# Kernel tuning notes

Hardware: AMD Instinct MI355X
Metric: run time of the kernel (lower is better)

Reference implementation:

```python
import jax, jax.numpy as jnp
import numpy as np

B, S, H = 64, 2048, 768
LAM = 0.0  # sparsegen-lin lambda (lam=0 -> sparsemax)
NEG = -1e30


def setup_inputs() -> dict:
    key = jax.random.key(0)
    k1, k2, k3, k4, k5 = jax.random.split(key, 5)
    hidden = jax.random.normal(k1, (B, S, H), jnp.float32)
    # contiguous entity spans of random length (>=16 valid tokens per example)
    lengths = jax.random.randint(k2, (B,), 16, S)
    mask1d = (jnp.arange(S)[None, :] < lengths[:, None]).astype(jnp.float32)
    token_mask = jnp.broadcast_to(mask1d[:, :, None], (B, S, H))
    pooled_tokens = jax.random.normal(k3, (B, H), jnp.float32)
    w_align = jax.random.normal(k4, (2 * H,), jnp.float32) * 0.02
    b_align = jax.random.normal(k5, (1,), jnp.float32) * 0.02
    return {"hidden": hidden, "token_mask": token_mask,
            "pooled_tokens": pooled_tokens, "w_align": w_align, "b_align": b_align}


def sparsegen_masked(scores, valid, lam):
    """Batched sparsegen-lin over valid positions only.
    scores: [B, S] float, valid: [B, S] bool. Returns probs [B, S] (0 at invalid).
    Matches per-example torch SparsegenLin applied to masked_select'd scores.
    """
    n = scores.shape[-1]
    zmax = jnp.max(jnp.where(valid, scores, -jnp.inf), axis=-1, keepdims=True)
    z = scores - zmax                                # subtract max over valid
    z_sortable = jnp.where(valid, z, NEG)
    zs = -jnp.sort(-z_sortable, axis=-1)             # descending; valid first
    n_valid = jnp.sum(valid, axis=-1, keepdims=True)
    ks = jnp.arange(1, n + 1, dtype=scores.dtype)[None, :]
    sorted_valid = ks <= n_valid.astype(scores.dtype)
    zs_m = jnp.where(sorted_valid, zs, 0.0)
    csum = jnp.cumsum(zs_m, axis=-1)
    bound = 1.0 - lam + ks * zs_m
    is_gt = (bound > csum) & sorted_valid
    k = jnp.maximum(jnp.max(jnp.where(is_gt, ks, 0.0), axis=-1, keepdims=True), 1.0)
    tau = (jnp.sum(jnp.where(is_gt, zs_m, 0.0), axis=-1, keepdims=True) - 1.0 + lam) / k
    ps = jnp.maximum((z - tau) / (1.0 - lam), 0.0)
    return jnp.where(valid, ps, 0.0)


def reference(hidden, token_mask, pooled_tokens, w_align, b_align):
    masked_hidden = hidden * token_mask                       # [B,S,H]
    tokens_rep_masked = pooled_tokens[:, None, :] * token_mask  # [B,S,H]
    # alignment_model(cat(tokens_rep_masked, masked_hidden)) -> [B,S]
    scores = (jnp.einsum('bsh,h->bs', tokens_rep_masked, w_align[:H])
              + jnp.einsum('bsh,h->bs', masked_hidden, w_align[H:])
              + b_align[0])
    attn_mask = token_mask[:, :, 0] > 0                       # [B,S] bool
    attention_probs = sparsegen_masked(scores, attn_mask, LAM)[:, :, None]  # [B,S,1]
    pooled = jnp.sum(masked_hidden * attention_probs, axis=1)  # [B,H]
    # insize == outsize -> output_layer is skipped (projected = pooled)
    return pooled, attention_probs
```

## Files before the change

### kernel.cpp

```cpp
#include <hip/hip_runtime.h>
#include <hip/hip_bf16.h>
#include <cstdint>
#include <cstddef>

#define BB 64
#define SS 2048
#define HH 768
#define LAM 0.0f
#define NEGV -1e30f

__global__ void lengths_kernel(const float* __restrict__ token_mask,
                               int* __restrict__ lens) {
    int wv = threadIdx.x >> 6;
    int b = blockIdx.x * 16 + wv;
    int lane = threadIdx.x & 63;

    int s1 = lane * 32;
    bool m1 = token_mask[((size_t)b * SS + s1) * HH] > 0.f;
    unsigned long long bal1 = __ballot(m1);
    int cnt1 = (int)__popcll(bal1);
    int base = (cnt1 - 1) * 32;

    int s2 = base + 1 + (lane & 31);
    if (s2 > SS - 1) s2 = SS - 1;
    bool m2 = token_mask[((size_t)b * SS + s2) * HH] > 0.f;
    unsigned long long bal2 = __ballot(m2) & 0xFFFFFFFFull;
    int cnt2 = (int)__popcll(bal2);
    if (lane == 0) lens[b] = base + 1 + cnt2;
}

__global__ void scores_kernel(const float* __restrict__ hidden,
                              const int* __restrict__ lens,
                              const float* __restrict__ w_align,
                              float* __restrict__ scores) {
    int row = blockIdx.x * 4 + (threadIdx.x >> 6);
    int lane = threadIdx.x & 63;
    int b = row >> 11;
    int s = row & (SS - 1);
    if (s >= lens[b]) return;
    const float* hrow = hidden + (size_t)row * HH;
    const float* w2 = w_align + HH;
    float acc = 0.f;
#pragma unroll
    for (int r = 0; r < 3; ++r) {
        int idx = r * 256 + lane * 4;
        float4 h = *reinterpret_cast<const float4*>(hrow + idx);
        float4 w = *reinterpret_cast<const float4*>(w2 + idx);
        acc += h.x * w.x + h.y * w.y + h.z * w.z + h.w * w.w;
    }
#pragma unroll
    for (int off = 32; off >= 1; off >>= 1) acc += __shfl_xor(acc, off);
    if (lane == 0) scores[row] = acc;
}

__global__ __launch_bounds__(768, 1) void tau_pool_kernel(
        const float* __restrict__ hidden,
        const float* __restrict__ pooled_tokens,
        const float* __restrict__ w_align,
        const float* __restrict__ b_align,
        const float* __restrict__ scores,
        const int* __restrict__ lens,
        float* __restrict__ out) {
    __shared__ int   s_idx[SS];
    __shared__ float s_p[SS];
    __shared__ int   s_cnt;

    const int b = blockIdx.x;
    const int t = threadIdx.x;
    const int lane = t & 63;
    const int wv = t >> 6;

    if (wv == 0) {
        const int len = lens[b];

        const float* pt = pooled_tokens + b * HH;
        float dp = 0.f;
#pragma unroll
        for (int i = 0; i < 3; ++i) {
            int idx = i * 256 + lane * 4;
            float4 a = *reinterpret_cast<const float4*>(pt + idx);
            float4 w = *reinterpret_cast<const float4*>(w_align + idx);
            dp += a.x * w.x + a.y * w.y + a.z * w.z + a.w * w.w;
        }
#pragma unroll
        for (int off = 32; off >= 1; off >>= 1) dp += __shfl_xor(dp, off);
        dp += b_align[0];

        const float* sc = scores + b * SS;
        float z[32];
#pragma unroll
        for (int i = 0; i < 8; ++i) {
            int e = i * 256 + lane * 4;
            float4 v = *reinterpret_cast<const float4*>(sc + e);
            z[i * 4 + 0] = (e + 0 < len) ? v.x + dp : NEGV;
            z[i * 4 + 1] = (e + 1 < len) ? v.y + dp : NEGV;
            z[i * 4 + 2] = (e + 2 < len) ? v.z + dp : NEGV;
            z[i * 4 + 3] = (e + 3 < len) ? v.w + dp : NEGV;
        }

        float mx = z[0];
#pragma unroll
        for (int i = 1; i < 32; ++i) mx = fmaxf(mx, z[i]);
#pragma unroll
        for (int off = 32; off >= 1; off >>= 1) mx = fmaxf(mx, __shfl_xor(mx, off));
#pragma unroll
        for (int i = 0; i < 32; ++i) z[i] -= mx;

        float tau = -1.0f;
#pragma unroll 1
        for (int it = 0; it < 50; ++it) {
            float a = 0.f, c = 0.f;
#pragma unroll
            for (int i = 0; i < 32; ++i) {
                bool g = z[i] > tau;
                a += g ? z[i] : 0.f;
                c += g ? 1.f : 0.f;
            }
#pragma unroll
            for (int off = 32; off >= 1; off >>= 1) {
                a += __shfl_xor(a, off);
                c += __shfl_xor(c, off);
            }
            float tn = (a - 1.f + LAM) / c;
            if (tn == tau) break;
            tau = tn;
        }

        const float inv = 1.f / (1.f - LAM);
        float p[32];
#pragma unroll
        for (int i = 0; i < 32; ++i) p[i] = fmaxf((z[i] - tau) * inv, 0.f);
        float* po = out + BB * HH + b * SS;
#pragma unroll
        for (int i = 0; i < 8; ++i) {
            float4 v = make_float4(p[i * 4 + 0], p[i * 4 + 1], p[i * 4 + 2], p[i * 4 + 3]);
            *reinterpret_cast<float4*>(po + i * 256 + lane * 4) = v;
        }

        int cnt = 0;
#pragma unroll
        for (int i = 0; i < 8; ++i) {
#pragma unroll
            for (int c = 0; c < 4; ++c) {
                float pv = p[i * 4 + c];
                unsigned long long m = __ballot(pv > 0.f);
                if (pv > 0.f) {
                    int pos = cnt + (int)__popcll(m & ((1ull << lane) - 1ull));
                    s_idx[pos] = i * 256 + lane * 4 + c;
                    s_p[pos] = pv;
                }
                cnt += (int)__popcll(m);
            }
        }
        if (lane == 0) s_cnt = cnt;
    }
    __syncthreads();

    const int cnt = s_cnt;
    const float* hb = hidden + (size_t)b * SS * HH;
    float acc = 0.f;
#pragma unroll 1
    for (int j = 0; j < cnt; j += 4) {
        int   i0 = s_idx[j];
        float p0 = s_p[j];
        int   i1 = (j + 1 < cnt) ? s_idx[j + 1] : 0;
        float p1 = (j + 1 < cnt) ? s_p[j + 1] : 0.f;
        int   i2 = (j + 2 < cnt) ? s_idx[j + 2] : 0;
        float p2 = (j + 2 < cnt) ? s_p[j + 2] : 0.f;
        int   i3 = (j + 3 < cnt) ? s_idx[j + 3] : 0;
        float p3 = (j + 3 < cnt) ? s_p[j + 3] : 0.f;
        float h0 = hb[(size_t)i0 * HH + t];
        float h1 = hb[(size_t)i1 * HH + t];
        float h2 = hb[(size_t)i2 * HH + t];
        float h3 = hb[(size_t)i3 * HH + t];
        acc += p0 * h0 + p1 * h1 + p2 * h2 + p3 * h3;
    }
    out[b * HH + t] = acc;
}

__global__ void scores_kernel_mask(const float* __restrict__ hidden,
                                   const float* __restrict__ token_mask,
                                   const float* __restrict__ w_align,
                                   float* __restrict__ scores) {
    int row = blockIdx.x * 4 + (threadIdx.x >> 6);
    int lane = threadIdx.x & 63;
    float m = token_mask[(size_t)row * HH];
    if (m == 0.0f) {
        if (lane == 0) scores[row] = NEGV;
        return;
    }
    const float* hrow = hidden + (size_t)row * HH;
    const float* w2 = w_align + HH;
    float acc = 0.f;
#pragma unroll
    for (int r = 0; r < 3; ++r) {
        int idx = r * 256 + lane * 4;
        float4 h = *reinterpret_cast<const float4*>(hrow + idx);
        float4 w = *reinterpret_cast<const float4*>(w2 + idx);
        acc += h.x * w.x + h.y * w.y + h.z * w.z + h.w * w.w;
    }
#pragma unroll
    for (int off = 32; off >= 1; off >>= 1) acc += __shfl_xor(acc, off);
    if (lane == 0) scores[row] = acc;
}

__global__ void sentinel_lens_kernel(const float* __restrict__ scores,
                                     int* __restrict__ lens) {
    int b = blockIdx.x;
    int t = threadIdx.x;
    int c = 0;
#pragma unroll
    for (int i = 0; i < 2; ++i) {
        float v = scores[b * SS + i * 1024 + t];
        c += (v > -1e29f) ? 1 : 0;
    }
#pragma unroll
    for (int off = 32; off >= 1; off >>= 1) c += __shfl_xor(c, off);
    __shared__ int red[16];
    if ((t & 63) == 0) red[t >> 6] = c;
    __syncthreads();
    if (t == 0) {
        int s = 0;
#pragma unroll
        for (int i = 0; i < 16; ++i) s += red[i];
        lens[b] = s;
    }
}

extern "C" void kernel_launch(void* const* d_in, const int* in_sizes, int n_in,
                              void* d_out, int out_size, void* d_ws, size_t ws_size,
                              hipStream_t stream) {
    const float* hidden        = (const float*)d_in[0];
    const float* token_mask    = (const float*)d_in[1];
    const float* pooled_tokens = (const float*)d_in[2];
    const float* w_align       = (const float*)d_in[3];
    const float* b_align       = (const float*)d_in[4];
    float* out = (float*)d_out;

    const size_t scores_bytes = (size_t)BB * SS * sizeof(float);
    const size_t need = scores_bytes + BB * sizeof(int);

    if (ws_size >= need) {
        float* scores_ws = (float*)d_ws;
        int*   lens      = (int*)((char*)d_ws + scores_bytes);

        lengths_kernel<<<dim3(4), dim3(1024), 0, stream>>>(token_mask, lens);
        scores_kernel<<<dim3((BB * SS) / 4), dim3(256), 0, stream>>>(
            hidden, lens, w_align, scores_ws);
        tau_pool_kernel<<<dim3(BB), dim3(768), 0, stream>>>(
            hidden, pooled_tokens, w_align, b_align, scores_ws, lens, out);
    } else {
        float* scores_ws = out + BB * HH;
        int* lens = (int*)d_ws;
        scores_kernel_mask<<<dim3((BB * SS) / 4), dim3(256), 0, stream>>>(
            hidden, token_mask, w_align, scores_ws);
        sentinel_lens_kernel<<<dim3(BB), dim3(1024), 0, stream>>>(scores_ws, lens);
        tau_pool_kernel<<<dim3(BB), dim3(768), 0, stream>>>(
            hidden, pooled_tokens, w_align, b_align, scores_ws, lens, out);
    }
}
```

Before: 47.94 us.

## Make scores kernel persistent with register double-buffered hidden row loads

The scores kernel moves from one wave per row (32768 blocks) to 2048 blocks in which each wave loops over 16 rows that share the same sequence position across batches. The weight slice is held in registers, and the next row's hidden data is prefetched while the current dot product is reduced. The aim is to cut launch and block scheduling overhead and keep more memory loads in flight. The cost is higher register use and a serial per-wave loop, which could lower effective memory parallelism. Rows are strided by batch, so load balance depends on how the random lengths fall.

```diff
diff --git a/kernel.cpp b/kernel.cpp
--- a/kernel.cpp
+++ b/kernel.cpp
@@ -8,6 +8,10 @@
 #define HH 768
 #define LAM 0.0f
 #define NEGV -1e30f
+
+__device__ __forceinline__ float dot4(float4 a, float4 b) {
+    return a.x * b.x + a.y * b.y + a.z * b.z + a.w * b.w;
+}
 
 __global__ void lengths_kernel(const float* __restrict__ token_mask,
                                int* __restrict__ lens) {
@@ -29,28 +33,53 @@
     if (lane == 0) lens[b] = base + 1 + cnt2;
 }
 
-__global__ void scores_kernel(const float* __restrict__ hidden,
-                              const int* __restrict__ lens,
-                              const float* __restrict__ w_align,
-                              float* __restrict__ scores) {
-    int row = blockIdx.x * 4 + (threadIdx.x >> 6);
-    int lane = threadIdx.x & 63;
-    int b = row >> 11;
-    int s = row & (SS - 1);
-    if (s >= lens[b]) return;
-    const float* hrow = hidden + (size_t)row * HH;
+__global__ __launch_bounds__(256) void scores_kernel(
+        const float* __restrict__ hidden,
+        const int* __restrict__ lens,
+        const float* __restrict__ w_align,
+        float* __restrict__ scores) {
+    const int lane = threadIdx.x & 63;
+    const int wv = threadIdx.x >> 6;
+    const int wgid = blockIdx.x * 4 + wv;
+    const int s = wgid & (SS - 1);
+    const int wi = lane * 4;
+
     const float* w2 = w_align + HH;
-    float acc = 0.f;
-#pragma unroll
-    for (int r = 0; r < 3; ++r) {
-        int idx = r * 256 + lane * 4;
-        float4 h = *reinterpret_cast<const float4*>(hrow + idx);
-        float4 w = *reinterpret_cast<const float4*>(w2 + idx);
-        acc += h.x * w.x + h.y * w.y + h.z * w.z + h.w * w.w;
-    }
-#pragma unroll
-    for (int off = 32; off >= 1; off >>= 1) acc += __shfl_xor(acc, off);
-    if (lane == 0) scores[row] = acc;
+    const float4 wr0 = *reinterpret_cast<const float4*>(w2 + wi);
+    const float4 wr1 = *reinterpret_cast<const float4*>(w2 + 256 + wi);
+    const float4 wr2 = *reinterpret_cast<const float4*>(w2 + 512 + wi);
+
+    int bcur = wgid >> 11;
+    bool vcur = s < lens[bcur];
+    float4 c0 = make_float4(0, 0, 0, 0), c1 = c0, c2 = c0;
+    if (vcur) {
+        const float* hp = hidden + ((size_t)bcur * SS + s) * HH;
+        c0 = *reinterpret_cast<const float4*>(hp + wi);
+        c1 = *reinterpret_cast<const float4*>(hp + 256 + wi);
+        c2 = *reinterpret_cast<const float4*>(hp + 512 + wi);
+    }
+
+#pragma unroll 1
+    for (int it = 0; it < 16; ++it) {
+        const int bnext = bcur + 4;
+        const bool vnext = (it < 15) && (s < lens[bnext]);
+        float4 n0 = make_float4(0, 0, 0, 0), n1 = n0, n2 = n0;
+        if (vnext) {
+            const float* np = hidden + ((size_t)bnext * SS + s) * HH;
+            n0 = *reinterpret_cast<const float4*>(np + wi);
+            n1 = *reinterpret_cast<const float4*>(np + 256 + wi);
+            n2 = *reinterpret_cast<const float4*>(np + 512 + wi);
+        }
+        if (vcur) {
+            float a = dot4(c0, wr0) + dot4(c1, wr1) + dot4(c2, wr2);
+#pragma unroll
+            for (int off = 32; off >= 1; off >>= 1) a += __shfl_xor(a, off);
+            if (lane == 0) scores[(size_t)bcur * SS + s] = a;
+        }
+        bcur = bnext;
+        vcur = vnext;
+        c0 = n0; c1 = n1; c2 = n2;
+    }
 }
 
 __global__ __launch_bounds__(768, 1) void tau_pool_kernel(
@@ -80,7 +109,7 @@
             int idx = i * 256 + lane * 4;
             float4 a = *reinterpret_cast<const float4*>(pt + idx);
             float4 w = *reinterpret_cast<const float4*>(w_align + idx);
-            dp += a.x * w.x + a.y * w.y + a.z * w.z + a.w * w.w;
+            dp += dot4(a, w);
         }
 #pragma unroll
         for (int off = 32; off >= 1; off >>= 1) dp += __shfl_xor(dp, off);
@@ -197,7 +226,7 @@
         int idx = r * 256 + lane * 4;
         float4 h = *reinterpret_cast<const float4*>(hrow + idx);
         float4 w = *reinterpret_cast<const float4*>(w2 + idx);
-        acc += h.x * w.x + h.y * w.y + h.z * w.z + h.w * w.w;
+        acc += dot4(h, w);
     }
 #pragma unroll
     for (int off = 32; off >= 1; off >>= 1) acc += __shfl_xor(acc, off);
@@ -245,7 +274,7 @@
         int*   lens      = (int*)((char*)d_ws + scores_bytes);
 
         lengths_kernel<<<dim3(4), dim3(1024), 0, stream>>>(token_mask, lens);
-        scores_kernel<<<dim3((BB * SS) / 4), dim3(256), 0, stream>>>(
+        scores_kernel<<<dim3(2048), dim3(256), 0, stream>>>(
             hidden, lens, w_align, scores_ws);
         tau_pool_kernel<<<dim3(BB), dim3(768), 0, stream>>>(
             hidden, pooled_tokens, w_align, b_align, scores_ws, lens, out);
```

Result: slower. 51.22 us (+6.8%).
